# Optimization experiments

Hardware: AMD Instinct MI355X
Metric: run time of the kernel (lower is better)

## Reference

```python
import jax, jax.numpy as jnp
import numpy as np

ROPE_BASE = 10000.0

def rotate_half(x):
    d = x.shape[-1] // 2
    return jnp.concatenate([-x[..., d:], x[..., :d]], axis=-1)

def rope_cos_sin(seq_len, head_dim, dtype=jnp.float32):
    inv_freq = 1.0 / (ROPE_BASE ** (jnp.arange(0, head_dim, 2, dtype=jnp.float32) / head_dim))
    t = jnp.arange(seq_len, dtype=jnp.float32)
    freqs = jnp.outer(t, inv_freq)              # [T, hd/2]
    emb = jnp.concatenate([freqs, freqs], axis=-1)  # [T, hd]
    return jnp.cos(emb).astype(dtype), jnp.sin(emb).astype(dtype)

def alibi_slopes(num_heads):
    return jnp.asarray([2.0 ** (-8.0 * i / num_heads) for i in range(1, num_heads + 1)], dtype=jnp.float32)

def setup_inputs() -> dict:
    key = jax.random.key(0)
    k1, k2, k3 = jax.random.split(key, 3)
    B, T, H = 2, 2048, 1024
    return {
        "q": jax.random.normal(k1, (B, T, H), dtype=jnp.float32),
        "k": jax.random.normal(k2, (B, T, H), dtype=jnp.float32),
        "v": jax.random.normal(k3, (B, T, H), dtype=jnp.float32),
        "num_heads": 16,
    }

def reference(q, k, v, num_heads):
    B, T, H = q.shape
    nh = num_heads
    hd = H // nh
    q = q.reshape(B, T, nh, hd)
    k = k.reshape(B, T, nh, hd)
    v = v.reshape(B, T, nh, hd)
    cos, sin = rope_cos_sin(T, hd, q.dtype)      # [T, hd]
    cos = cos[None, :, None, :]                  # [1, T, 1, hd]
    sin = sin[None, :, None, :]
    q = q * cos + rotate_half(q) * sin
    k = k * cos + rotate_half(k) * sin
    # ALiBi additive bias: [nh, T, T]
    rel = jnp.arange(T)[None, :] - jnp.arange(T)[:, None]   # memory - context
    bias = alibi_slopes(nh)[:, None, None] * rel.astype(q.dtype)
    scale = 1.0 / jnp.sqrt(jnp.asarray(hd, dtype=q.dtype))
    scores = jnp.einsum('bqhd,bkhd->bhqk', q, k) * scale + bias[None]
    attn = jax.nn.softmax(scores, axis=-1)
    out = jnp.einsum('bhqk,bkhd->bqhd', attn, v)
    return out.reshape(B, T, H)
```

## Files before the change

kernel.cpp:

```cpp
#include <hip/hip_runtime.h>
#include <math.h>

#define TB 2
#define TT 2048
#define NH 16
#define HD 64
#define HSZ 1024
#define NROW 65536
#define OPHALF 4194304

typedef float floatx4 __attribute__((ext_vector_type(4)));
typedef __bf16 bf16x4 __attribute__((ext_vector_type(4)));
typedef __bf16 bf16x8 __attribute__((ext_vector_type(8)));

#define LOG2E  1.4426950408889634f
#define NEGF   (-0.4152410118609203f)
#define INV2PI 0.15915494309189535f

__global__ __launch_bounds__(256)
void prep_kernel(const float* __restrict__ K, const float* __restrict__ V,
                 __bf16* __restrict__ Kp, __bf16* __restrict__ Vp) {
    int blk = blockIdx.x;
    int kt = blk & 31;
    int bh = blk >> 5;
    int b = bh >> 4, h = bh & 15;
    int tid = threadIdx.x;

    {
        int key = tid >> 2, qq = tid & 3;
        int tglob = kt * 64 + key;
        const float* krow = K + ((size_t)(b * TT + tglob)) * HSZ + h * HD + qq * 8;
        float x0[8], x1[8];
        *(floatx4*)&x0[0] = *(const floatx4*)&krow[0];
        *(floatx4*)&x0[4] = *(const floatx4*)&krow[4];
        *(floatx4*)&x1[0] = *(const floatx4*)&krow[32];
        *(floatx4*)&x1[4] = *(const floatx4*)&krow[36];
        bf16x8 y0, y1;
        #pragma unroll
        for (int j = 0; j < 8; ++j) {
            float freq = exp2f((float)(qq * 8 + j) * NEGF);
            float rv = (float)tglob * freq * INV2PI;
            rv -= floorf(rv);
            float s = __builtin_amdgcn_sinf(rv);
            float c = __builtin_amdgcn_cosf(rv);
            y0[j] = (__bf16)(x0[j] * c - x1[j] * s);
            y1[j] = (__bf16)(x1[j] * c + x0[j] * s);
        }
        size_t base = ((size_t)blk * 4 + (key & 3)) * 1024 + (size_t)(qq * 16 + (key >> 2)) * 8;
        *(bf16x8*)(Kp + base)       = y0;
        *(bf16x8*)(Kp + base + 512) = y1;
    }

    __shared__ __bf16 lt[64][72];
    {
        int vkey = tid >> 2, dg = (tid & 3) * 16;
        const float* vrow = V + ((size_t)(b * TT + kt * 64 + vkey)) * HSZ + h * HD + dg;
        floatx4 v0 = *(const floatx4*)&vrow[0];
        floatx4 v1 = *(const floatx4*)&vrow[4];
        floatx4 v2 = *(const floatx4*)&vrow[8];
        floatx4 v3 = *(const floatx4*)&vrow[12];
        #pragma unroll
        for (int j = 0; j < 4; ++j) {
            lt[dg + j][vkey]      = (__bf16)v0[j];
            lt[dg + 4 + j][vkey]  = (__bf16)v1[j];
            lt[dg + 8 + j][vkey]  = (__bf16)v2[j];
            lt[dg + 12 + j][vkey] = (__bf16)v3[j];
        }
    }
    __syncthreads();
    #pragma unroll
    for (int ss = 0; ss < 2; ++ss) {
        int s = tid + ss * 256;
        int hg = s >> 6;
        int l = s & 63;
        int lq = l >> 4, lr = l & 15;
        int h2 = hg >> 2, g = hg & 3;
        bf16x8 o = *(const bf16x8*)&lt[g * 16 + lr][h2 * 32 + lq * 8];
        *(bf16x8*)(Vp + (size_t)blk * 4096 + (size_t)hg * 512 + (size_t)l * 8) = o;
    }
}

__global__ __launch_bounds__(256, 2)
void attn_kernel(const float* __restrict__ Q, const __bf16* __restrict__ Kp,
                 const __bf16* __restrict__ Vp, __bf16* __restrict__ Op,
                 float* __restrict__ lp) {
    int blk0 = blockIdx.x;
    int blk = (blk0 & 7) * 128 + (blk0 >> 3);

    int s = blk & 1;
    int qb = (blk >> 1) & 15;
    int bh = blk >> 5;
    int b = bh >> 4, h = bh & 15;
    int tid = threadIdx.x;
    int wave = tid >> 6, lane = tid & 63;
    int lane15 = lane & 15, quad = lane >> 4;

    __shared__ __align__(16) __bf16 sP[4][2][16][72];

    const float scale2 = 0.125f * LOG2E;
    const float slope2 = exp2f(-0.5f * (float)(h + 1)) * LOG2E;
    const float ms     = slope2 * 2047.0f + 20.0f;

    int qbase = qb * 128 + wave * 32;
    int d0 = quad * 8;
    bf16x8 aQ0[2], aQ1[2];
    #pragma unroll
    for (int qf = 0; qf < 2; ++qf) {
        int t_q = qbase + qf * 16 + lane15;
        const float* qrow = Q + ((size_t)(b * TT + t_q) * HSZ) + h * HD;
        float q0[8], q1[8];
        *(floatx4*)&q0[0] = *(const floatx4*)&qrow[d0];
        *(floatx4*)&q0[4] = *(const floatx4*)&qrow[d0 + 4];
        *(floatx4*)&q1[0] = *(const floatx4*)&qrow[d0 + 32];
        *(floatx4*)&q1[4] = *(const floatx4*)&qrow[d0 + 36];
        #pragma unroll
        for (int j = 0; j < 8; ++j) {
            float freq = exp2f((float)(d0 + j) * NEGF);
            float rv = (float)t_q * freq * INV2PI;
            rv -= floorf(rv);
            float sn = __builtin_amdgcn_sinf(rv);
            float cs = __builtin_amdgcn_cosf(rv);
            aQ0[qf][j] = (__bf16)((q0[j] * cs - q1[j] * sn) * scale2);
            aQ1[qf][j] = (__bf16)((q1[j] * cs + q0[j] * sn) * scale2);
        }
    }

    float slk2[4];
    #pragma unroll
    for (int nt = 0; nt < 4; ++nt)
        slk2[nt] = slope2 * (float)(4 * lane15 + nt) - ms;
    const float dstep = slope2 * 64.0f;

    floatx4 O[2][4];
    float lrow[2][4];
    #pragma unroll
    for (int qf = 0; qf < 2; ++qf)
        #pragma unroll
        for (int r = 0; r < 4; ++r) {
            O[qf][r] = (floatx4){0.f, 0.f, 0.f, 0.f};
            lrow[qf][r] = 0.f;
        }

    const __bf16* Kb = Kp + (size_t)bh * (TT * HD) + (size_t)lane * 8;
    const __bf16* Vb = Vp + (size_t)bh * (TT * HD) + (size_t)lane * 8;

    const int kt0 = s * 16, kt1 = s * 16 + 16;

    bf16x8 bk[4][2];
    {
        const __bf16* kbase = Kb + (size_t)kt0 * 4096;
        #pragma unroll
        for (int nt = 0; nt < 4; ++nt) {
            bk[nt][0] = *(const bf16x8*)(kbase + nt * 1024);
            bk[nt][1] = *(const bf16x8*)(kbase + nt * 1024 + 512);
        }
    }

    #pragma unroll 1
    for (int kt = kt0; kt < kt1; ++kt) {
        const __bf16* vbase = Vb + (size_t)kt * 4096;
        bf16x8 bv[2][4];
        #pragma unroll
        for (int hg = 0; hg < 8; ++hg)
            bv[hg >> 2][hg & 3] = *(const bf16x8*)(vbase + hg * 512);

        float biask = dstep * (float)kt;
        #pragma unroll
        for (int qf = 0; qf < 2; ++qf) {
            float P[4][4];
            #pragma unroll
            for (int nt = 0; nt < 4; ++nt) {
                floatx4 acc = {0.f, 0.f, 0.f, 0.f};
                acc = __builtin_amdgcn_mfma_f32_16x16x32_bf16(aQ0[qf], bk[nt][0], acc, 0, 0, 0);
                acc = __builtin_amdgcn_mfma_f32_16x16x32_bf16(aQ1[qf], bk[nt][1], acc, 0, 0, 0);
                float bias = slk2[nt] + biask;
                #pragma unroll
                for (int r = 0; r < 4; ++r)
                    P[nt][r] = __builtin_amdgcn_exp2f(acc[r] + bias);
            }
            #pragma unroll
            for (int r = 0; r < 4; ++r) {
                lrow[qf][r] += (P[0][r] + P[1][r]) + (P[2][r] + P[3][r]);
                bf16x4 pp;
                pp[0] = (__bf16)P[0][r]; pp[1] = (__bf16)P[1][r];
                pp[2] = (__bf16)P[2][r]; pp[3] = (__bf16)P[3][r];
                *(bf16x4*)&sP[wave][qf][quad * 4 + r][4 * lane15] = pp;
            }
        }

        if (kt + 1 < kt1) {
            const __bf16* kbase = Kb + (size_t)(kt + 1) * 4096;
            #pragma unroll
            for (int nt = 0; nt < 4; ++nt) {
                bk[nt][0] = *(const bf16x8*)(kbase + nt * 1024);
                bk[nt][1] = *(const bf16x8*)(kbase + nt * 1024 + 512);
            }
        }

        #pragma unroll
        for (int qf = 0; qf < 2; ++qf) {
            #pragma unroll
            for (int h2 = 0; h2 < 2; ++h2) {
                bf16x8 aP = *(const bf16x8*)&sP[wave][qf][lane15][h2 * 32 + quad * 8];
                O[qf][0] = __builtin_amdgcn_mfma_f32_16x16x32_bf16(aP, bv[h2][0], O[qf][0], 0, 0, 0);
                O[qf][1] = __builtin_amdgcn_mfma_f32_16x16x32_bf16(aP, bv[h2][1], O[qf][1], 0, 0, 0);
                O[qf][2] = __builtin_amdgcn_mfma_f32_16x16x32_bf16(aP, bv[h2][2], O[qf][2], 0, 0, 0);
                O[qf][3] = __builtin_amdgcn_mfma_f32_16x16x32_bf16(aP, bv[h2][3], O[qf][3], 0, 0, 0);
            }
        }
    }

    #pragma unroll
    for (int qf = 0; qf < 2; ++qf) {
        int q_glb = qbase + qf * 16 + quad * 4;
        #pragma unroll
        for (int r = 0; r < 4; ++r) {
            float l = lrow[qf][r];
            l += __shfl_xor(l, 1);
            l += __shfl_xor(l, 2);
            l += __shfl_xor(l, 4);
            l += __shfl_xor(l, 8);
            int rid = (b * TT + q_glb + r) * NH + h;
            size_t base = ((size_t)s * NROW + rid) * HD + lane15;
            Op[base +  0] = (__bf16)O[qf][0][r];
            Op[base + 16] = (__bf16)O[qf][1][r];
            Op[base + 32] = (__bf16)O[qf][2][r];
            Op[base + 48] = (__bf16)O[qf][3][r];
            if (lane15 == 0) lp[s * NROW + rid] = l;
        }
    }
}

__global__ __launch_bounds__(256)
void reduce_kernel(const __bf16* __restrict__ Op, const float* __restrict__ lp,
                   float* __restrict__ Out) {
    int i = blockIdx.x * 256 + threadIdx.x;
    size_t f = (size_t)i * 4;
    int rid = (int)(f >> 6);
    bf16x4 a = *(const bf16x4*)(Op + f);
    bf16x4 c = *(const bf16x4*)(Op + OPHALF + f);
    float inv = 1.0f / (lp[rid] + lp[NROW + rid]);
    floatx4 o;
    #pragma unroll
    for (int j = 0; j < 4; ++j)
        o[j] = ((float)a[j] + (float)c[j]) * inv;
    *(floatx4*)(Out + f) = o;
}

extern "C" void kernel_launch(void* const* d_in, const int* in_sizes, int n_in,
                              void* d_out, int out_size, void* d_ws, size_t ws_size,
                              hipStream_t stream) {
    const float* q = (const float*)d_in[0];
    const float* k = (const float*)d_in[1];
    const float* v = (const float*)d_in[2];
    float* out = (float*)d_out;

    char* ws = (char*)d_ws;
    __bf16* Kp = (__bf16*)ws;
    __bf16* Vp = (__bf16*)(ws + (size_t)8 * 1024 * 1024);
    __bf16* Op = (__bf16*)(ws + (size_t)16 * 1024 * 1024);
    float*  lp = (float*)(ws + (size_t)33 * 1024 * 1024);

    prep_kernel<<<dim3(TB * NH * (TT / 64)), 256, 0, stream>>>(k, v, Kp, Vp);
    attn_kernel<<<dim3(TB * NH * 32), 256, 0, stream>>>(q, Kp, Vp, Op, lp);
    reduce_kernel<<<dim3((TB * TT * HSZ / 4) / 256), 256, 0, stream>>>(Op, lp, out);
}
```

Measured before the change: 144.7 us.

## Compute transposed QK^T to keep P in registers and skip LDS round-trip

```diff
diff --git a/kernel.cpp b/kernel.cpp
--- a/kernel.cpp
+++ b/kernel.cpp
@@ -70,12 +70,12 @@
     __syncthreads();
     #pragma unroll
     for (int ss = 0; ss < 2; ++ss) {
-        int s = tid + ss * 256;
-        int hg = s >> 6;
-        int l = s & 63;
+        int sidx = tid + ss * 256;
+        int hg = sidx >> 6;
+        int l = sidx & 63;
+        int g = hg >> 2, dn = hg & 3;
         int lq = l >> 4, lr = l & 15;
-        int h2 = hg >> 2, g = hg & 3;
-        bf16x8 o = *(const bf16x8*)&lt[g * 16 + lr][h2 * 32 + lq * 8];
+        bf16x8 o = *(const bf16x8*)&lt[dn * 16 + lr][lq * 16 + g * 8];
         *(bf16x8*)(Vp + (size_t)blk * 4096 + (size_t)hg * 512 + (size_t)l * 8) = o;
     }
 }
@@ -94,8 +94,6 @@
     int tid = threadIdx.x;
     int wave = tid >> 6, lane = tid & 63;
     int lane15 = lane & 15, quad = lane >> 4;
-
-    __shared__ __align__(16) __bf16 sP[4][2][16][72];
 
     const float scale2 = 0.125f * LOG2E;
     const float slope2 = exp2f(-0.5f * (float)(h + 1)) * LOG2E;
@@ -125,21 +123,18 @@
         }
     }
 
-    float slk2[4];
-    #pragma unroll
-    for (int nt = 0; nt < 4; ++nt)
-        slk2[nt] = slope2 * (float)(4 * lane15 + nt) - ms;
+    const float qb16  = slope2 * (float)(16 * quad) - ms;
     const float dstep = slope2 * 64.0f;
 
     floatx4 O[2][4];
-    float lrow[2][4];
-    #pragma unroll
-    for (int qf = 0; qf < 2; ++qf)
-        #pragma unroll
-        for (int r = 0; r < 4; ++r) {
+    float lrow[2];
+    #pragma unroll
+    for (int qf = 0; qf < 2; ++qf) {
+        lrow[qf] = 0.f;
+        #pragma unroll
+        for (int r = 0; r < 4; ++r)
             O[qf][r] = (floatx4){0.f, 0.f, 0.f, 0.f};
-            lrow[qf][r] = 0.f;
-        }
+    }
 
     const __bf16* Kb = Kp + (size_t)bh * (TT * HD) + (size_t)lane * 8;
     const __bf16* Vb = Vp + (size_t)bh * (TT * HD) + (size_t)lane * 8;
@@ -164,69 +159,95 @@
         for (int hg = 0; hg < 8; ++hg)
             bv[hg >> 2][hg & 3] = *(const bf16x8*)(vbase + hg * 512);
 
-        float biask = dstep * (float)kt;
-        #pragma unroll
-        for (int qf = 0; qf < 2; ++qf) {
-            float P[4][4];
+        float biasq = qb16 + dstep * (float)kt;
+
+        {
+            floatx4 acc[4];
             #pragma unroll
             for (int nt = 0; nt < 4; ++nt) {
-                floatx4 acc = {0.f, 0.f, 0.f, 0.f};
-                acc = __builtin_amdgcn_mfma_f32_16x16x32_bf16(aQ0[qf], bk[nt][0], acc, 0, 0, 0);
-                acc = __builtin_amdgcn_mfma_f32_16x16x32_bf16(aQ1[qf], bk[nt][1], acc, 0, 0, 0);
-                float bias = slk2[nt] + biask;
+                floatx4 a = {0.f, 0.f, 0.f, 0.f};
+                a = __builtin_amdgcn_mfma_f32_16x16x32_bf16(bk[nt][0], aQ0[0], a, 0, 0, 0);
+                a = __builtin_amdgcn_mfma_f32_16x16x32_bf16(bk[nt][1], aQ1[0], a, 0, 0, 0);
+                acc[nt] = a;
+            }
+            #pragma unroll
+            for (int g = 0; g < 2; ++g) {
+                bf16x8 aP;
+                float ps = 0.f;
                 #pragma unroll
-                for (int r = 0; r < 4; ++r)
-                    P[nt][r] = __builtin_amdgcn_exp2f(acc[r] + bias);
-            }
-            #pragma unroll
-            for (int r = 0; r < 4; ++r) {
-                lrow[qf][r] += (P[0][r] + P[1][r]) + (P[2][r] + P[3][r]);
-                bf16x4 pp;
-                pp[0] = (__bf16)P[0][r]; pp[1] = (__bf16)P[1][r];
-                pp[2] = (__bf16)P[2][r]; pp[3] = (__bf16)P[3][r];
-                *(bf16x4*)&sP[wave][qf][quad * 4 + r][4 * lane15] = pp;
-            }
-        }
-
-        if (kt + 1 < kt1) {
-            const __bf16* kbase = Kb + (size_t)(kt + 1) * 4096;
+                for (int j = 0; j < 8; ++j) {
+                    int nt = j & 3, r = g * 2 + (j >> 2);
+                    float p = __builtin_amdgcn_exp2f(
+                        acc[nt][r] + fmaf(slope2, (float)(4 * r + nt), biasq));
+                    ps += p;
+                    aP[j] = (__bf16)p;
+                }
+                lrow[0] += ps;
+                O[0][0] = __builtin_amdgcn_mfma_f32_16x16x32_bf16(aP, bv[g][0], O[0][0], 0, 0, 0);
+                O[0][1] = __builtin_amdgcn_mfma_f32_16x16x32_bf16(aP, bv[g][1], O[0][1], 0, 0, 0);
+                O[0][2] = __builtin_amdgcn_mfma_f32_16x16x32_bf16(aP, bv[g][2], O[0][2], 0, 0, 0);
+                O[0][3] = __builtin_amdgcn_mfma_f32_16x16x32_bf16(aP, bv[g][3], O[0][3], 0, 0, 0);
+            }
+        }
+
+        {
+            floatx4 acc[4];
             #pragma unroll
             for (int nt = 0; nt < 4; ++nt) {
-                bk[nt][0] = *(const bf16x8*)(kbase + nt * 1024);
-                bk[nt][1] = *(const bf16x8*)(kbase + nt * 1024 + 512);
-            }
-        }
-
-        #pragma unroll
-        for (int qf = 0; qf < 2; ++qf) {
-            #pragma unroll
-            for (int h2 = 0; h2 < 2; ++h2) {
-                bf16x8 aP = *(const bf16x8*)&sP[wave][qf][lane15][h2 * 32 + quad * 8];
-                O[qf][0] = __builtin_amdgcn_mfma_f32_16x16x32_bf16(aP, bv[h2][0], O[qf][0], 0, 0, 0);
-                O[qf][1] = __builtin_amdgcn_mfma_f32_16x16x32_bf16(aP, bv[h2][1], O[qf][1], 0, 0, 0);
-                O[qf][2] = __builtin_amdgcn_mfma_f32_16x16x32_bf16(aP, bv[h2][2], O[qf][2], 0, 0, 0);
-                O[qf][3] = __builtin_amdgcn_mfma_f32_16x16x32_bf16(aP, bv[h2][3], O[qf][3], 0, 0, 0);
+                floatx4 a = {0.f, 0.f, 0.f, 0.f};
+                a = __builtin_amdgcn_mfma_f32_16x16x32_bf16(bk[nt][0], aQ0[1], a, 0, 0, 0);
+                a = __builtin_amdgcn_mfma_f32_16x16x32_bf16(bk[nt][1], aQ1[1], a, 0, 0, 0);
+                acc[nt] = a;
+            }
+
+            if (kt + 1 < kt1) {
+                const __bf16* kbase = Kb + (size_t)(kt + 1) * 4096;
+                #pragma unroll
+                for (int nt = 0; nt < 4; ++nt) {
+                    bk[nt][0] = *(const bf16x8*)(kbase + nt * 1024);
+                    bk[nt][1] = *(const bf16x8*)(kbase + nt * 1024 + 512);
+                }
+            }
+
+            #pragma unroll
+            for (int g = 0; g < 2; ++g) {
+                bf16x8 aP;
+                float ps = 0.f;
+                #pragma unroll
+                for (int j = 0; j < 8; ++j) {
+                    int nt = j & 3, r = g * 2 + (j >> 2);
+                    float p = __builtin_amdgcn_exp2f(
+                        acc[nt][r] + fmaf(slope2, (float)(4 * r + nt), biasq));
+                    ps += p;
+                    aP[j] = (__bf16)p;
+                }
+                lrow[1] += ps;
+                O[1][0] = __builtin_amdgcn_mfma_f32_16x16x32_bf16(aP, bv[g][0], O[1][0], 0, 0, 0);
+                O[1][1] = __builtin_amdgcn_mfma_f32_16x16x32_bf16(aP, bv[g][1], O[1][1], 0, 0, 0);
+                O[1][2] = __builtin_amdgcn_mfma_f32_16x16x32_bf16(aP, bv[g][2], O[1][2], 0, 0, 0);
+                O[1][3] = __builtin_amdgcn_mfma_f32_16x16x32_bf16(aP, bv[g][3], O[1][3], 0, 0, 0);
             }
         }
     }
 
     #pragma unroll
     for (int qf = 0; qf < 2; ++qf) {
-        int q_glb = qbase + qf * 16 + quad * 4;
+        float l = lrow[qf];
+        l += __shfl_xor(l, 16);
+        l += __shfl_xor(l, 32);
+        int q0 = qbase + qf * 16;
+        if (quad == 0) {
+            int ridl = (b * TT + q0 + lane15) * NH + h;
+            lp[s * NROW + ridl] = l;
+        }
         #pragma unroll
         for (int r = 0; r < 4; ++r) {
-            float l = lrow[qf][r];
-            l += __shfl_xor(l, 1);
-            l += __shfl_xor(l, 2);
-            l += __shfl_xor(l, 4);
-            l += __shfl_xor(l, 8);
-            int rid = (b * TT + q_glb + r) * NH + h;
+            int rid = (b * TT + q0 + quad * 4 + r) * NH + h;
             size_t base = ((size_t)s * NROW + rid) * HD + lane15;
             Op[base +  0] = (__bf16)O[qf][0][r];
             Op[base + 16] = (__bf16)O[qf][1][r];
             Op[base + 32] = (__bf16)O[qf][2][r];
             Op[base + 48] = (__bf16)O[qf][3][r];
-            if (lane15 == 0) lp[s * NROW + rid] = l;
         }
     }
 }
```

Result: no change. 144.0 us (-0.5%).

## Drop split-K attention and reduce kernel, normalize output in attention kernel

Applied to the files above, without the earlier changes.

```diff
diff --git a/kernel.cpp b/kernel.cpp
--- a/kernel.cpp
+++ b/kernel.cpp
@@ -6,8 +6,6 @@
 #define NH 16
 #define HD 64
 #define HSZ 1024
-#define NROW 65536
-#define OPHALF 4194304
 
 typedef float floatx4 __attribute__((ext_vector_type(4)));
 typedef __bf16 bf16x4 __attribute__((ext_vector_type(4)));
@@ -82,14 +80,12 @@
 
 __global__ __launch_bounds__(256, 2)
 void attn_kernel(const float* __restrict__ Q, const __bf16* __restrict__ Kp,
-                 const __bf16* __restrict__ Vp, __bf16* __restrict__ Op,
-                 float* __restrict__ lp) {
+                 const __bf16* __restrict__ Vp, float* __restrict__ Out) {
     int blk0 = blockIdx.x;
-    int blk = (blk0 & 7) * 128 + (blk0 >> 3);
-
-    int s = blk & 1;
-    int qb = (blk >> 1) & 15;
-    int bh = blk >> 5;
+    int blk = (blk0 & 7) * 64 + (blk0 >> 3);
+
+    int qb = blk & 15;
+    int bh = blk >> 4;
     int b = bh >> 4, h = bh & 15;
     int tid = threadIdx.x;
     int wave = tid >> 6, lane = tid & 63;
@@ -144,11 +140,11 @@
     const __bf16* Kb = Kp + (size_t)bh * (TT * HD) + (size_t)lane * 8;
     const __bf16* Vb = Vp + (size_t)bh * (TT * HD) + (size_t)lane * 8;
 
-    const int kt0 = s * 16, kt1 = s * 16 + 16;
+    const int kt1 = TT / 64;
 
     bf16x8 bk[4][2];
     {
-        const __bf16* kbase = Kb + (size_t)kt0 * 4096;
+        const __bf16* kbase = Kb;
         #pragma unroll
         for (int nt = 0; nt < 4; ++nt) {
             bk[nt][0] = *(const bf16x8*)(kbase + nt * 1024);
@@ -157,7 +153,7 @@
     }
 
     #pragma unroll 1
-    for (int kt = kt0; kt < kt1; ++kt) {
+    for (int kt = 0; kt < kt1; ++kt) {
         const __bf16* vbase = Vb + (size_t)kt * 4096;
         bf16x8 bv[2][4];
         #pragma unroll
@@ -212,7 +208,6 @@
 
     #pragma unroll
     for (int qf = 0; qf < 2; ++qf) {
-        int q_glb = qbase + qf * 16 + quad * 4;
         #pragma unroll
         for (int r = 0; r < 4; ++r) {
             float l = lrow[qf][r];
@@ -220,31 +215,15 @@
             l += __shfl_xor(l, 2);
             l += __shfl_xor(l, 4);
             l += __shfl_xor(l, 8);
-            int rid = (b * TT + q_glb + r) * NH + h;
-            size_t base = ((size_t)s * NROW + rid) * HD + lane15;
-            Op[base +  0] = (__bf16)O[qf][0][r];
-            Op[base + 16] = (__bf16)O[qf][1][r];
-            Op[base + 32] = (__bf16)O[qf][2][r];
-            Op[base + 48] = (__bf16)O[qf][3][r];
-            if (lane15 == 0) lp[s * NROW + rid] = l;
-        }
-    }
-}
-
-__global__ __launch_bounds__(256)
-void reduce_kernel(const __bf16* __restrict__ Op, const float* __restrict__ lp,
-                   float* __restrict__ Out) {
-    int i = blockIdx.x * 256 + threadIdx.x;
-    size_t f = (size_t)i * 4;
-    int rid = (int)(f >> 6);
-    bf16x4 a = *(const bf16x4*)(Op + f);
-    bf16x4 c = *(const bf16x4*)(Op + OPHALF + f);
-    float inv = 1.0f / (lp[rid] + lp[NROW + rid]);
-    floatx4 o;
-    #pragma unroll
-    for (int j = 0; j < 4; ++j)
-        o[j] = ((float)a[j] + (float)c[j]) * inv;
-    *(floatx4*)(Out + f) = o;
+            float inv = 1.0f / l;
+            int t = qbase + qf * 16 + quad * 4 + r;
+            size_t base = ((size_t)(b * TT + t)) * HSZ + h * HD + lane15;
+            Out[base +  0] = O[qf][0][r] * inv;
+            Out[base + 16] = O[qf][1][r] * inv;
+            Out[base + 32] = O[qf][2][r] * inv;
+            Out[base + 48] = O[qf][3][r] * inv;
+        }
+    }
 }
 
 extern "C" void kernel_launch(void* const* d_in, const int* in_sizes, int n_in,
@@ -258,10 +237,7 @@
     char* ws = (char*)d_ws;
     __bf16* Kp = (__bf16*)ws;
     __bf16* Vp = (__bf16*)(ws + (size_t)8 * 1024 * 1024);
-    __bf16* Op = (__bf16*)(ws + (size_t)16 * 1024 * 1024);
-    float*  lp = (float*)(ws + (size_t)33 * 1024 * 1024);
 
     prep_kernel<<<dim3(TB * NH * (TT / 64)), 256, 0, stream>>>(k, v, Kp, Vp);
-    attn_kernel<<<dim3(TB * NH * 32), 256, 0, stream>>>(q, Kp, Vp, Op, lp);
-    reduce_kernel<<<dim3((TB * TT * HSZ / 4) / 256), 256, 0, stream>>>(Op, lp, out);
+    attn_kernel<<<dim3(TB * NH * 16), 256, 0, stream>>>(q, Kp, Vp, out);
 }
```

New measurement: 136.9 us. 5.4% less time.
